# Kernel optimization log

Measured on AMD Instinct MI355X. Metric: run time of the kernel, lower is better.

Reference implementation:

```python
import jax, jax.numpy as jnp
import numpy as np

B, S, D_IN, D_OUT = 1, 2048, 4096, 4096
N_HEADS, N_KV = 32, 8
HEAD_DIM = D_OUT // N_HEADS  # 128
GROUP = N_HEADS // N_KV      # 4


def _rope_tables(seq_len, head_dim, base=10000.0):
    inv = 1.0 / (base ** (np.arange(0, head_dim, 2, dtype=np.float32) / head_dim))
    t = np.arange(seq_len, dtype=np.float32)
    ang = np.outer(t, inv)                       # [S, hd/2]
    ang = np.concatenate([ang, ang], axis=-1)    # [S, hd]
    return jnp.asarray(np.cos(ang)), jnp.asarray(np.sin(ang))


def setup_inputs() -> dict:
    key = jax.random.key(0)
    kx, kq, kk, kv, ko = jax.random.split(key, 5)
    cos, sin = _rope_tables(S, HEAD_DIM)
    sc = 0.02
    return {
        "x": jax.random.normal(kx, (B, S, D_IN), dtype=jnp.float32),
        "cos": cos,
        "sin": sin,
        "Wq": jax.random.normal(kq, (D_OUT, D_IN), dtype=jnp.float32) * sc,
        "Wk": jax.random.normal(kk, (N_KV * HEAD_DIM, D_IN), dtype=jnp.float32) * sc,
        "Wv": jax.random.normal(kv, (N_KV * HEAD_DIM, D_IN), dtype=jnp.float32) * sc,
        "Wo": jax.random.normal(ko, (D_OUT, D_OUT), dtype=jnp.float32) * sc,
    }


def _apply_rope(t, cos, sin):
    # t: [b, h, s, hd]; cos/sin: [s, hd] -> rotate-half RoPE
    hd = t.shape[-1]
    x1, x2 = t[..., : hd // 2], t[..., hd // 2 :]
    rotated = jnp.concatenate([-x2, x1], axis=-1)
    return t * cos[None, None] + rotated * sin[None, None]


def reference(x, cos, sin, Wq, Wk, Wv, Wo):
    b, s, _ = x.shape
    q = (x @ Wq.T).reshape(b, s, N_HEADS, HEAD_DIM).transpose(0, 2, 1, 3)  # [b,H,s,hd]
    k = (x @ Wk.T).reshape(b, s, N_KV, HEAD_DIM).transpose(0, 2, 1, 3)     # [b,G,s,hd]
    v = (x @ Wv.T).reshape(b, s, N_KV, HEAD_DIM).transpose(0, 2, 1, 3)
    q = _apply_rope(q, cos, sin)
    k = _apply_rope(k, cos, sin)
    k = jnp.repeat(k, GROUP, axis=1)  # [b,H,s,hd]
    v = jnp.repeat(v, GROUP, axis=1)
    scores = jnp.einsum("bhqd,bhkd->bhqk", q, k)
    causal = jnp.triu(jnp.ones((s, s), dtype=bool), k=1)
    scores = jnp.where(causal[None, None], -jnp.inf, scores)
    attn = jax.nn.softmax(scores / jnp.sqrt(jnp.float32(HEAD_DIM)), axis=-1)
    ctx = jnp.einsum("bhqk,bhkd->bhqd", attn, v)
    ctx = ctx.transpose(0, 2, 1, 3).reshape(b, s, D_OUT)
    return ctx @ Wo.T
```

## Files before the change

kernel.cpp:

```cpp
#include <hip/hip_runtime.h>


typedef __bf16 bf16;
typedef __bf16 bf16x4 __attribute__((ext_vector_type(4)));
typedef __bf16 bf16x8 __attribute__((ext_vector_type(8)));
typedef float  f32x4  __attribute__((ext_vector_type(4)));

#define S_LEN   2048
#define DMODEL  4096
#define QKV_N   6144
#define K_OFF   4096
#define V_OFF   5120
#define HD      128
#define ATT_SCALE 0.08838834764831845f

__device__ __forceinline__ void gload16(const bf16* g, bf16* l) {
    __builtin_amdgcn_global_load_lds(
        (__attribute__((address_space(1))) void*)(g),
        (__attribute__((address_space(3))) void*)(l),
        16, 0, 0);
}

__global__ __launch_bounds__(256) void cast_f32_bf16(const float* __restrict__ in,
                                                     bf16* __restrict__ out, int n4) {
    int i = blockIdx.x * 256 + threadIdx.x;
    if (i >= n4) return;
    float4 v = reinterpret_cast<const float4*>(in)[i];
    bf16x4 o;
    o[0] = (bf16)v.x; o[1] = (bf16)v.y; o[2] = (bf16)v.z; o[3] = (bf16)v.w;
    reinterpret_cast<bf16x4*>(out)[i] = o;
}

template <typename OutT>
__global__ __launch_bounds__(512, 2) void gemm256(const bf16* __restrict__ A,
                                                  const bf16* __restrict__ B,
                                                  OutT* __restrict__ C,
                                                  int M, int N, int K, int ldc) {
    __shared__ bf16 Lsh[2 * 2 * 256 * 64];
    const int t    = threadIdx.x;
    const int lane = t & 63;
    const int wave = t >> 6;
    const int quad = lane >> 4, l15 = lane & 15;
    const int wm = wave >> 2, wn = wave & 3;

    int bid = blockIdx.y * gridDim.x + blockIdx.x;
    const int nwg = gridDim.x * gridDim.y;
    {
        const int q = nwg >> 3, r = nwg & 7;
        const int x = bid & 7, i = bid >> 3;
        bid = (x < r ? x * (q + 1) : r * (q + 1) + (x - r) * q) + i;
    }
    const int ntm = M >> 8;
    const int bm  = (bid % ntm) << 8;
    const int bn  = (bid / ntm) << 8;

    const bf16* Ablk = A + (size_t)bm * K;
    const bf16* Bblk = B + (size_t)bn * K;
    const int NT = K >> 6;

    bf16* L0A = Lsh;
    bf16* L0B = Lsh + 16384;
    bf16* L1A = Lsh + 32768;
    bf16* L1B = Lsh + 49152;

    {
        #define STAGE_HALF(G, LR)                                              \
            {                                                                  \
                _Pragma("unroll")                                              \
                for (int j = 0; j < 2; ++j) {                                  \
                    const int r = j * 64 + (t >> 3);                           \
                    const int c = ((t & 7) ^ ((t >> 3) & 7)) << 3;             \
                    gload16((G) + (size_t)r * K + c,                           \
                            (LR) + j * 4096 + ((t >> 6) << 9));                \
                }                                                              \
            }
        STAGE_HALF(Ablk,                    L0A);
        STAGE_HALF(Ablk + (size_t)128 * K,  L0A + 8192);
        STAGE_HALF(Bblk,                    L0B);
        STAGE_HALF(Bblk + (size_t)128 * K,  L0B + 8192);
        if (NT > 1) {
            STAGE_HALF(Bblk + 64,                   L1B);
            STAGE_HALF(Bblk + (size_t)128 * K + 64, L1B + 8192);
        }
        asm volatile("s_waitcnt vmcnt(0)" ::: "memory");
        __builtin_amdgcn_s_barrier();
    }

    f32x4 acc[8][4];
#pragma unroll
    for (int i = 0; i < 8; ++i)
#pragma unroll
        for (int j = 0; j < 4; ++j) acc[i][j] = (f32x4){0.f, 0.f, 0.f, 0.f};

    for (int tile = 0; tile < NT; ++tile) {
        bf16* As = (tile & 1) ? L1A : L0A;
        bf16* Bs = (tile & 1) ? L1B : L0B;
        bf16* An = (tile & 1) ? L0A : L1A;
        bf16x8 bfr[4][2];
#pragma unroll
        for (int q = 0; q < 4; ++q) {
            bf16x8 af[2][2];
#pragma unroll
            for (int dm = 0; dm < 2; ++dm)
#pragma unroll
                for (int kk = 0; kk < 2; ++kk) {
                    const int row = wm * 128 + q * 32 + dm * 16 + l15;
                    const int ch  = (kk * 4 + quad) ^ (row & 7);
                    af[dm][kk] = *reinterpret_cast<const bf16x8*>(
                        &As[row * 64 + (ch << 3)]);
                }
            if (q == 0) {
#pragma unroll
                for (int n = 0; n < 4; ++n)
#pragma unroll
                    for (int kk = 0; kk < 2; ++kk) {
                        const int row = wn * 64 + n * 16 + l15;
                        const int ch  = (kk * 4 + quad) ^ (row & 7);
                        bfr[n][kk] = *reinterpret_cast<const bf16x8*>(
                            &Bs[row * 64 + (ch << 3)]);
                    }
                if (tile + 1 < NT)
                    STAGE_HALF(Ablk + (size_t)(tile + 1) * 64, An);
            } else if (q == 1) {
                if (tile + 1 < NT)
                    STAGE_HALF(Ablk + (size_t)128 * K + (size_t)(tile + 1) * 64,
                               An + 8192);
                if (tile + 2 < NT)
                    STAGE_HALF(Bblk + (size_t)(tile + 2) * 64, Bs);
            } else if (q == 2) {
                if (tile + 2 < NT)
                    STAGE_HALF(Bblk + (size_t)128 * K + (size_t)(tile + 2) * 64,
                               Bs + 8192);
            }
            __builtin_amdgcn_s_barrier();
            asm volatile("s_waitcnt lgkmcnt(0)" ::: "memory");
            __builtin_amdgcn_s_setprio(1);
#pragma unroll
            for (int dm = 0; dm < 2; ++dm)
#pragma unroll
                for (int n = 0; n < 4; ++n)
#pragma unroll
                    for (int kk = 0; kk < 2; ++kk)
                        acc[q * 2 + dm][n] = __builtin_amdgcn_mfma_f32_16x16x32_bf16(
                            af[dm][kk], bfr[n][kk], acc[q * 2 + dm][n], 0, 0, 0);
            __builtin_amdgcn_s_setprio(0);
            if (q < 3) {
                __builtin_amdgcn_s_barrier();
            } else {
                if (tile < NT - 2) { asm volatile("s_waitcnt vmcnt(4)" ::: "memory"); }
                else               { asm volatile("s_waitcnt vmcnt(0)" ::: "memory"); }
                __builtin_amdgcn_s_barrier();
            }
        }
    }
    #undef STAGE_HALF

#pragma unroll
    for (int mf = 0; mf < 8; ++mf) {
        const int row0 = bm + wm * 128 + mf * 16 + quad * 4;
#pragma unroll
        for (int nf = 0; nf < 4; ++nf) {
            const int col = bn + wn * 64 + nf * 16 + l15;
#pragma unroll
            for (int r = 0; r < 4; ++r)
                C[(size_t)(row0 + r) * ldc + col] = (OutT)acc[mf][nf][r];
        }
    }
}

__global__ __launch_bounds__(256) void rope_kernel(bf16* __restrict__ qkv,
                                                   const float* __restrict__ cosT,
                                                   const float* __restrict__ sinT) {
    const int col = blockIdx.x * 256 + threadIdx.x;
    if (col >= 40 * 64) return;
    const int row  = blockIdx.y;
    const int head = col >> 6, d = col & 63;
    const size_t base = (size_t)row * QKV_N + head * 128 + d;
    const float x1 = (float)qkv[base];
    const float x2 = (float)qkv[base + 64];
    const float c  = cosT[row * 128 + d];
    const float s  = sinT[row * 128 + d];
    qkv[base]      = (bf16)(x1 * c - x2 * s);
    qkv[base + 64] = (bf16)(x2 * c + x1 * s);
}

__global__ __launch_bounds__(256) void transpose_v(const bf16* __restrict__ qkv,
                                                   bf16* __restrict__ vt) {
    __shared__ bf16 T[64][72];
    const int c0 = blockIdx.x * 64;
    const int s0 = blockIdx.y * 64;
    const int t  = threadIdx.x;
#pragma unroll
    for (int it = 0; it < 2; ++it) {
        const int sl = (t >> 3) + it * 32;
        const int c8 = (t & 7) * 8;
        bf16x8 v = *reinterpret_cast<const bf16x8*>(
            qkv + (size_t)(s0 + sl) * QKV_N + V_OFF + c0 + c8);
        *reinterpret_cast<bf16x8*>(&T[sl][c8]) = v;
    }
    __syncthreads();
#pragma unroll
    for (int it = 0; it < 2; ++it) {
        const int cl = (t >> 3) + it * 32;
        const int s8 = (t & 7) * 8;
        bf16x8 o;
#pragma unroll
        for (int e = 0; e < 8; ++e) o[e] = T[s8 + e][cl];
        *reinterpret_cast<bf16x8*>(vt + (size_t)(c0 + cl) * S_LEN + s0 + s8) = o;
    }
}

__global__ __launch_bounds__(512) void flash_attn(const bf16* __restrict__ qkv,
                                                  const bf16* __restrict__ vt,
                                                  bf16* __restrict__ ctx) {
    const int blk   = blockIdx.x;
    const int qtile = 15 - (blk >> 5);
    const int h     = blk & 31;
    const int kh    = h >> 2;
    const int q0    = qtile * 128;
    const int t     = threadIdx.x;
    const int wave  = t >> 6, lane = t & 63;
    const int quad  = lane >> 4, l15 = lane & 15;

    __shared__ bf16 Ks[64 * 128];
    __shared__ bf16 Vs[128 * 64];
    __shared__ bf16 Ps[8 * 16 * 72];

    const bf16* Qb  = qkv + h * HD;
    const bf16* Kb  = qkv + K_OFF + kh * HD;
    const bf16* Vth = vt + (size_t)kh * HD * S_LEN;

    const int qrow_a = q0 + wave * 16 + l15;
    bf16x8 qf[4];
#pragma unroll
    for (int kk = 0; kk < 4; ++kk)
        qf[kk] = *reinterpret_cast<const bf16x8*>(
            Qb + (size_t)qrow_a * QKV_N + kk * 32 + quad * 8);

    float m_i[4], l_i[4];
    f32x4 o_acc[8];
#pragma unroll
    for (int r = 0; r < 4; ++r) { m_i[r] = -1e30f; l_i[r] = 0.f; }
#pragma unroll
    for (int dt = 0; dt < 8; ++dt) o_acc[dt] = (f32x4){0.f, 0.f, 0.f, 0.f};

    const int myrow = q0 + wave * 16 + quad * 4;
    bf16* PsW = Ps + wave * (16 * 72);

    for (int kv0 = 0; kv0 < q0 + 128; kv0 += 64) {
        __syncthreads();
#pragma unroll
        for (int it = 0; it < 2; ++it) {
            const int rb = wave * 8 + it * 4;
            const int r  = rb + (lane >> 4);
            const int cg = (lane & 15) ^ (r & 15);
            gload16(Kb + (size_t)(kv0 + r) * QKV_N + cg * 8, Ks + rb * 128);
        }
#pragma unroll
        for (int it = 0; it < 2; ++it) {
            const int db = wave * 16 + it * 8;
            const int d  = db + (lane >> 3);
            const int cg = (lane & 7) ^ (d & 7);
            gload16(Vth + (size_t)d * S_LEN + kv0 + cg * 8, Vs + db * 64);
        }
        __syncthreads();

        float sv[4][4];
        const bool need_mask = (kv0 + 63) > q0;
#pragma unroll
        for (int j = 0; j < 4; ++j) {
            f32x4 s = (f32x4){0.f, 0.f, 0.f, 0.f};
#pragma unroll
            for (int kk = 0; kk < 4; ++kk) {
                const int cd = kk * 4 + quad;
                bf16x8 kf = *reinterpret_cast<const bf16x8*>(
                    &Ks[(j * 16 + l15) * 128 + ((cd ^ l15) & 15) * 8]);
                s = __builtin_amdgcn_mfma_f32_16x16x32_bf16(qf[kk], kf, s, 0, 0, 0);
            }
            if (need_mask) {
#pragma unroll
                for (int r = 0; r < 4; ++r)
                    sv[j][r] = ((kv0 + j * 16 + l15) <= (myrow + r))
                                   ? s[r] * ATT_SCALE : -1e30f;
            } else {
#pragma unroll
                for (int r = 0; r < 4; ++r) sv[j][r] = s[r] * ATT_SCALE;
            }
        }

        float al[4];
#pragma unroll
        for (int r = 0; r < 4; ++r) {
            float mt = fmaxf(fmaxf(sv[0][r], sv[1][r]), fmaxf(sv[2][r], sv[3][r]));
#pragma unroll
            for (int off = 1; off < 16; off <<= 1) mt = fmaxf(mt, __shfl_xor(mt, off));
            const float mn = fmaxf(m_i[r], mt);
            al[r] = __expf(m_i[r] - mn);
            m_i[r] = mn;
            float rs = 0.f;
#pragma unroll
            for (int j = 0; j < 4; ++j) {
                const float p = __expf(sv[j][r] - mn);
                rs += p;
                PsW[(quad * 4 + r) * 72 + j * 16 + l15] = (bf16)p;
            }
#pragma unroll
            for (int off = 1; off < 16; off <<= 1) rs += __shfl_xor(rs, off);
            l_i[r] = l_i[r] * al[r] + rs;
        }

#pragma unroll
        for (int dt = 0; dt < 8; ++dt) {
            o_acc[dt][0] *= al[0]; o_acc[dt][1] *= al[1];
            o_acc[dt][2] *= al[2]; o_acc[dt][3] *= al[3];
        }

        bf16x8 pa[2];
        pa[0] = *reinterpret_cast<const bf16x8*>(&PsW[l15 * 72 + quad * 8]);
        pa[1] = *reinterpret_cast<const bf16x8*>(&PsW[l15 * 72 + 32 + quad * 8]);
#pragma unroll
        for (int dt = 0; dt < 8; ++dt) {
#pragma unroll
            for (int c = 0; c < 2; ++c) {
                const int ck = c * 4 + quad;
                bf16x8 vb = *reinterpret_cast<const bf16x8*>(
                    &Vs[(dt * 16 + l15) * 64 + ((ck ^ (l15 & 7)) & 7) * 8]);
                o_acc[dt] = __builtin_amdgcn_mfma_f32_16x16x32_bf16(pa[c], vb, o_acc[dt], 0, 0, 0);
            }
        }
    }

#pragma unroll
    for (int dt = 0; dt < 8; ++dt)
#pragma unroll
        for (int r = 0; r < 4; ++r)
            ctx[(size_t)(myrow + r) * DMODEL + h * HD + dt * 16 + l15] =
                (bf16)(o_acc[dt][r] / l_i[r]);
}

extern "C" void kernel_launch(void* const* d_in, const int* in_sizes, int n_in,
                              void* d_out, int out_size, void* d_ws, size_t ws_size,
                              hipStream_t stream) {
    const float* x    = (const float*)d_in[0];
    const float* cosT = (const float*)d_in[1];
    const float* sinT = (const float*)d_in[2];
    const float* Wq   = (const float*)d_in[3];
    const float* Wk   = (const float*)d_in[4];
    const float* Wv   = (const float*)d_in[5];
    const float* Wo   = (const float*)d_in[6];
    float* out = (float*)d_out;

    bf16* xb   = (bf16*)d_ws;
    bf16* Wqkv = xb   + (size_t)S_LEN * DMODEL;
    bf16* Wob  = Wqkv + (size_t)QKV_N * DMODEL;
    bf16* QKV  = Wob  + (size_t)DMODEL * DMODEL;
    bf16* ctx  = QKV  + (size_t)S_LEN * QKV_N;
    bf16* Vt   = ctx  + (size_t)S_LEN * DMODEL;

    cast_f32_bf16<<<(S_LEN * DMODEL / 4 + 255) / 256, 256, 0, stream>>>(x, xb, S_LEN * DMODEL / 4);
    cast_f32_bf16<<<(DMODEL * DMODEL / 4 + 255) / 256, 256, 0, stream>>>(Wq, Wqkv, DMODEL * DMODEL / 4);
    cast_f32_bf16<<<(1024 * DMODEL / 4 + 255) / 256, 256, 0, stream>>>(
        Wk, Wqkv + (size_t)4096 * DMODEL, 1024 * DMODEL / 4);
    cast_f32_bf16<<<(1024 * DMODEL / 4 + 255) / 256, 256, 0, stream>>>(
        Wv, Wqkv + (size_t)5120 * DMODEL, 1024 * DMODEL / 4);
    cast_f32_bf16<<<(DMODEL * DMODEL / 4 + 255) / 256, 256, 0, stream>>>(Wo, Wob, DMODEL * DMODEL / 4);

    gemm256<bf16><<<dim3(QKV_N / 256, S_LEN / 256), 512, 0, stream>>>(
        xb, Wqkv, QKV, S_LEN, QKV_N, DMODEL, QKV_N);

    rope_kernel<<<dim3(10, S_LEN), 256, 0, stream>>>(QKV, cosT, sinT);

    transpose_v<<<dim3(16, 32), 256, 0, stream>>>(QKV, Vt);

    flash_attn<<<dim3(16 * 32), 512, 0, stream>>>(QKV, Vt, ctx);

    gemm256<float><<<dim3(DMODEL / 256, S_LEN / 256), 512, 0, stream>>>(
        ctx, Wob, out, S_LEN, DMODEL, DMODEL, DMODEL);
}
```

Measured before the change: 554.7 us.

## Use templated 128x256 tile GEMM with XCD-aware block remap for output projection

Adds a templated GEMM kernel with configurable tile size, an XCD-aware block-index remapping, split prefetch of A and B tiles, and launch bounds allowing two blocks per CU. The output projection now uses 128x256 tiles, doubling the grid from 128 to 256 workgroups so more of the GPU's compute units are busy. The trade-off is lower data reuse per tile and a more intricate wait-count schedule that could stall or go wrong if the vmcnt values do not match the outstanding loads.

```diff
diff --git a/kernel.cpp b/kernel.cpp
--- a/kernel.cpp
+++ b/kernel.cpp
@@ -168,6 +168,157 @@
     }
 }
 
+template <typename OutT, int MF, int NF>
+__global__ __launch_bounds__(512, 2) void gemmT(const bf16* __restrict__ A,
+                                                const bf16* __restrict__ B,
+                                                OutT* __restrict__ C,
+                                                int M, int N, int K, int ldc) {
+    constexpr int BM = MF * 32, BN = NF * 64;
+    constexpr int nA = BM / 64, nB = BN / 64;
+    constexpr int TU = nA + nB;
+    constexpr int CEIL = (TU + 2) / 3;
+    constexpr int AE = BM * 64, BE = BN * 64;
+    constexpr int MPP = MF / 4;
+
+    __shared__ bf16 Lsh[2 * (AE + BE)];
+    const int t    = threadIdx.x;
+    const int lane = t & 63;
+    const int quad = lane >> 4, l15 = lane & 15;
+    const int wave = t >> 6;
+    const int wm = wave >> 2, wn = wave & 3;
+
+    int bid = blockIdx.y * gridDim.x + blockIdx.x;
+    const int nwg = gridDim.x * gridDim.y;
+    {
+        const int q = nwg >> 3, r = nwg & 7;
+        const int x = bid & 7, i = bid >> 3;
+        bid = (x < r ? x * (q + 1) : r * (q + 1) + (x - r) * q) + i;
+    }
+    const int ntm = M / BM;
+    const int bm  = (bid % ntm) * BM;
+    const int bn  = (bid / ntm) * BN;
+
+    const bf16* Ablk = A + (size_t)bm * K;
+    const bf16* Bblk = B + (size_t)bn * K;
+    const int NT = K >> 6;
+
+    bf16* L0A = Lsh;
+    bf16* L0B = Lsh + AE;
+    bf16* L1A = Lsh + AE + BE;
+    bf16* L1B = L1A + AE;
+
+    const int urow = t >> 3;
+    const int csw  = ((t & 7) ^ (urow & 7)) << 3;
+    const int wbase = (t >> 6) << 9;
+
+    {
+#pragma unroll
+        for (int u = 0; u < nA; ++u)
+            gload16(Ablk + (size_t)(u * 64 + urow) * K + csw, L0A + u * 4096 + wbase);
+#pragma unroll
+        for (int u = 0; u < nB; ++u)
+            gload16(Bblk + (size_t)(u * 64 + urow) * K + csw, L0B + u * 4096 + wbase);
+        if (NT > 1) {
+#pragma unroll
+            for (int u = 0; u < nB; ++u)
+                gload16(Bblk + (size_t)(u * 64 + urow) * K + 64 + csw,
+                        L1B + u * 4096 + wbase);
+        }
+        asm volatile("s_waitcnt vmcnt(0)" ::: "memory");
+        __builtin_amdgcn_s_barrier();
+    }
+
+    f32x4 acc[MF][NF];
+#pragma unroll
+    for (int i = 0; i < MF; ++i)
+#pragma unroll
+        for (int j = 0; j < NF; ++j) acc[i][j] = (f32x4){0.f, 0.f, 0.f, 0.f};
+
+    for (int tile = 0; tile < NT; ++tile) {
+        bf16* As = (tile & 1) ? L1A : L0A;
+        bf16* Bs = (tile & 1) ? L1B : L0B;
+        bf16* An = (tile & 1) ? L0A : L1A;
+        bf16x8 bfr[NF][2];
+#pragma unroll
+        for (int q = 0; q < 4; ++q) {
+            bf16x8 af[MPP][2];
+#pragma unroll
+            for (int dm = 0; dm < MPP; ++dm)
+#pragma unroll
+                for (int kk = 0; kk < 2; ++kk) {
+                    const int row = wm * (MF * 16) + q * (MPP * 16) + dm * 16 + l15;
+                    const int ch  = (kk * 4 + quad) ^ (row & 7);
+                    af[dm][kk] = *reinterpret_cast<const bf16x8*>(
+                        &As[row * 64 + (ch << 3)]);
+                }
+            if (q == 0) {
+#pragma unroll
+                for (int n = 0; n < NF; ++n)
+#pragma unroll
+                    for (int kk = 0; kk < 2; ++kk) {
+                        const int row = wn * (NF * 16) + n * 16 + l15;
+                        const int ch  = (kk * 4 + quad) ^ (row & 7);
+                        bfr[n][kk] = *reinterpret_cast<const bf16x8*>(
+                            &Bs[row * 64 + (ch << 3)]);
+                    }
+            }
+            if (q < 3) {
+#pragma unroll
+                for (int u = 0; u < TU; ++u) {
+                    if (u / CEIL == q) {
+                        if (u < nA) {
+                            if (tile + 1 < NT)
+                                gload16(Ablk + (size_t)(u * 64 + urow) * K +
+                                            (tile + 1) * 64 + csw,
+                                        An + u * 4096 + wbase);
+                        } else {
+                            if (tile + 2 < NT)
+                                gload16(Bblk + (size_t)((u - nA) * 64 + urow) * K +
+                                            (tile + 2) * 64 + csw,
+                                        Bs + (u - nA) * 4096 + wbase);
+                        }
+                    }
+                }
+            }
+            __builtin_amdgcn_s_barrier();
+            asm volatile("s_waitcnt lgkmcnt(0)" ::: "memory");
+            __builtin_amdgcn_s_setprio(1);
+#pragma unroll
+            for (int dm = 0; dm < MPP; ++dm)
+#pragma unroll
+                for (int n = 0; n < NF; ++n)
+#pragma unroll
+                    for (int kk = 0; kk < 2; ++kk)
+                        acc[q * MPP + dm][n] = __builtin_amdgcn_mfma_f32_16x16x32_bf16(
+                            af[dm][kk], bfr[n][kk], acc[q * MPP + dm][n], 0, 0, 0);
+            __builtin_amdgcn_s_setprio(0);
+            if (q < 3) {
+                __builtin_amdgcn_s_barrier();
+            } else {
+                if (tile < NT - 2) {
+                    if constexpr (nB == 3) { asm volatile("s_waitcnt vmcnt(3)" ::: "memory"); }
+                    else                   { asm volatile("s_waitcnt vmcnt(4)" ::: "memory"); }
+                } else {
+                    asm volatile("s_waitcnt vmcnt(0)" ::: "memory");
+                }
+                __builtin_amdgcn_s_barrier();
+            }
+        }
+    }
+
+#pragma unroll
+    for (int mf = 0; mf < MF; ++mf) {
+        const int row0 = bm + wm * (MF * 16) + mf * 16 + quad * 4;
+#pragma unroll
+        for (int nf = 0; nf < NF; ++nf) {
+            const int col = bn + wn * (NF * 16) + nf * 16 + l15;
+#pragma unroll
+            for (int r = 0; r < 4; ++r)
+                C[(size_t)(row0 + r) * ldc + col] = (OutT)acc[mf][nf][r];
+        }
+    }
+}
+
 __global__ __launch_bounds__(256) void rope_kernel(bf16* __restrict__ qkv,
                                                    const float* __restrict__ cosT,
                                                    const float* __restrict__ sinT) {
@@ -374,6 +525,6 @@
 
     flash_attn<<<dim3(16 * 32), 512, 0, stream>>>(QKV, Vt, ctx);
 
-    gemm256<float><<<dim3(DMODEL / 256, S_LEN / 256), 512, 0, stream>>>(
+    gemmT<float, 4, 4><<<dim3(DMODEL / 256, S_LEN / 128), 512, 0, stream>>>(
         ctx, Wob, out, S_LEN, DMODEL, DMODEL, DMODEL);
 }
```

Result: faster. 516.7 us (-6.8%).
